# Kernel optimization log

Hardware: AMD Instinct MI355X
Metric: run time of the kernel (lower is better)

## Reference

```python
import jax, jax.numpy as jnp
import numpy as np
import math

NUM_HEADS = 16
HEAD_SIZE = 64
HIDDEN = NUM_HEADS * HEAD_SIZE
LN_EPS = 1e-12


def setup_inputs() -> dict:
    key = jax.random.key(0)
    ks = jax.random.split(key, 8)
    B, Lw, Le, H = 8, 512, 64, HIDDEN
    scale = 0.02
    return {
        "word_hidden_states": jax.random.normal(ks[0], (B, Lw, H), jnp.float32),
        "entity_hidden_states": jax.random.normal(ks[1], (B, Le, H), jnp.float32),
        "attention_mask": jnp.zeros((B, 1, 1, Lw + Le), jnp.float32),
        "Wq": jax.random.normal(ks[2], (H, H), jnp.float32) * scale,
        "bq": jnp.zeros((H,), jnp.float32),
        "Wk": jax.random.normal(ks[3], (H, H), jnp.float32) * scale,
        "bk": jnp.zeros((H,), jnp.float32),
        "Wv": jax.random.normal(ks[4], (H, H), jnp.float32) * scale,
        "bv": jnp.zeros((H,), jnp.float32),
        "Wo": jax.random.normal(ks[5], (H, H), jnp.float32) * scale,
        "bo": jnp.zeros((H,), jnp.float32),
        "ln_w": jnp.ones((H,), jnp.float32),
        "ln_b": jnp.zeros((H,), jnp.float32),
    }


def _layernorm(x, w, b):
    u = jnp.mean(x, axis=-1, keepdims=True)
    s = jnp.mean(jnp.square(x - u), axis=-1, keepdims=True)
    return w * ((x - u) / jnp.sqrt(s + LN_EPS)) + b


def reference(word_hidden_states, entity_hidden_states, attention_mask,
              Wq, bq, Wk, bk, Wv, bv, Wo, bo, ln_w, ln_b):
    B, Lw, H = word_hidden_states.shape
    x = jnp.concatenate([word_hidden_states, entity_hidden_states], axis=1)  # [B,S,H]
    S = x.shape[1]

    def heads(t):  # [B,S,H] -> [B,nh,S,hd]
        return t.reshape(B, S, NUM_HEADS, HEAD_SIZE).transpose(0, 2, 1, 3)

    q = heads(x @ Wq + bq)
    k = heads(x @ Wk + bk)
    v = heads(x @ Wv + bv)

    scores = jnp.einsum("bhqd,bhkd->bhqk", q, k) / math.sqrt(HEAD_SIZE)
    scores = scores + attention_mask  # additive mask, broadcast [B,1,1,S]
    probs = jax.nn.softmax(scores, axis=-1)
    ctx = jnp.einsum("bhqk,bhkd->bhqd", probs, v)
    ctx = ctx.transpose(0, 2, 1, 3).reshape(B, S, H)

    # SelfOutput (shared weights) applied per-stream; equivalent on concat since
    # residual is the concatenated input and LayerNorm is per-token.
    out = _layernorm(ctx @ Wo + bo + x, ln_w, ln_b)
    return out[:, :Lw, :], out[:, Lw:, :]
```

## Files before the change

### kernel.cpp

```cpp
#include <hip/hip_runtime.h>

#define NHEADS 16
#define HDIM   64
#define HID    1024
#define BATCH  8
#define LW     512
#define LE     64
#define SEQ    576
#define MTOT   (BATCH * SEQ)

typedef unsigned short u16;
typedef __bf16 bf16x8 __attribute__((ext_vector_type(8)));
typedef float  f32x4  __attribute__((ext_vector_type(4)));

__device__ __forceinline__ u16 f2bf(float f) {
  union { float f; unsigned int i; } x;
  x.f = f;
  unsigned int u = x.i;
  unsigned int r = (u + 0x7FFFu + ((u >> 16) & 1u)) >> 16;
  return (u16)r;
}
__device__ __forceinline__ unsigned int pk2(float a, float b) {
  return (unsigned int)f2bf(a) | ((unsigned int)f2bf(b) << 16);
}

__device__ __forceinline__ void gload16(const u16* g, u16* l) {
  __builtin_amdgcn_global_load_lds(
      (const __attribute__((address_space(1))) void*)g,
      (__attribute__((address_space(3))) void*)l, 16, 0, 0);
}

__global__ __launch_bounds__(256) void prep_k(
    const float* __restrict__ w0, const float* __restrict__ w1,
    const float* __restrict__ w2, const float* __restrict__ w3,
    u16* __restrict__ wt,
    const float* __restrict__ word, const float* __restrict__ ent,
    u16* __restrict__ xb)
{
  const int bid = blockIdx.x, tid = threadIdx.x;
  if (bid < 4096) {
    __shared__ u16 tile[32][33];
    const int z = bid >> 10, rem = bid & 1023;
    const int bx = rem & 31, by = rem >> 5;
    const float* src = (z == 0) ? w0 : (z == 1) ? w1 : (z == 2) ? w2 : w3;
    u16* dst = wt + (size_t)z * HID * HID;
    const int tx = tid & 31, ty = tid >> 5;
    const int nx = bx * 32, ky = by * 32;
#pragma unroll
    for (int j = 0; j < 4; ++j)
      tile[ty * 4 + j][tx] = f2bf(src[(size_t)(ky + ty * 4 + j) * HID + nx + tx]);
    __syncthreads();
#pragma unroll
    for (int j = 0; j < 4; ++j)
      dst[(size_t)(nx + ty * 4 + j) * HID + ky + tx] = tile[tx][ty * 4 + j];
  } else {
    const int row = bid - 4096;
    const int bb = row / SEQ, ss = row - bb * SEQ;
    const float* src = (ss < LW) ? word + (size_t)(bb * LW + ss) * HID
                                 : ent  + (size_t)(bb * LE + (ss - LW)) * HID;
    float4 v = *(const float4*)(src + tid * 4);
    ushort4 o;
    o.x = f2bf(v.x); o.y = f2bf(v.y); o.z = f2bf(v.z); o.w = f2bf(v.w);
    *(ushort4*)(xb + (size_t)row * HID + tid * 4) = o;
  }
}

__global__ __launch_bounds__(256) void qkv_gemm_k(
    const u16* __restrict__ xb, const u16* __restrict__ wt,
    const float* __restrict__ bq, const float* __restrict__ bk, const float* __restrict__ bv,
    u16* __restrict__ q_ws, u16* __restrict__ k_ws, u16* __restrict__ v_ws)
{
  __shared__ u16 sh[4 * 64 * 68];
  const int which = blockIdx.z;
  const u16* W = wt + (size_t)which * HID * HID;
  const float* bias = (which == 0) ? bq : (which == 1) ? bk : bv;
  const int m0 = blockIdx.x * 128, n0 = blockIdx.y * 128;
  const int tid = threadIdx.x, lane = tid & 63, wv = tid >> 6;
  const int lr = lane & 15, quad = lane >> 4;
  const int wm = (wv >> 1) * 64, wn = (wv & 1) * 64;

  const int subrow = lane >> 3;
  const int gsw = ((lane & 7) ^ subrow) * 8;
  const int fsw = lr & 7;

  u16* As = sh;
  u16* Bs = sh + 8192;

  const f32x4 fz = {0.f, 0.f, 0.f, 0.f};
  f32x4 acc[4][4];
#pragma unroll
  for (int a = 0; a < 4; ++a)
#pragma unroll
    for (int b = 0; b < 4; ++b) acc[a][b] = fz;

  for (int ki = 0; ki < 16; ++ki) {
    const int k0 = ki * 64;
#pragma unroll
    for (int j = 0; j < 4; ++j) {
      int row = (wv * 4 + j) * 8 + subrow;
      u16* ldst = sh + ((wv * 4 + j) * 64 + lane) * 8;
      gload16(xb + (size_t)(m0 + row) * HID + k0 + gsw, ldst);
      gload16(W  + (size_t)(n0 + row) * HID + k0 + gsw, ldst + 8192);
    }
    __syncthreads();
#pragma unroll
    for (int ks = 0; ks < 2; ++ks) {
      bf16x8 af[4], bfr[4];
#pragma unroll
      for (int i = 0; i < 4; ++i) {
        af[i]  = *(const bf16x8*)(&As[(wm + i * 16 + lr) * 64 + (((ks * 4 + quad) ^ fsw) * 8)]);
        bfr[i] = *(const bf16x8*)(&Bs[(wn + i * 16 + lr) * 64 + (((ks * 4 + quad) ^ fsw) * 8)]);
      }
      if (which < 2) {
#pragma unroll
        for (int a = 0; a < 4; ++a)
#pragma unroll
          for (int b = 0; b < 4; ++b)
            acc[a][b] = __builtin_amdgcn_mfma_f32_16x16x32_bf16(bfr[a], af[b], acc[a][b], 0, 0, 0);
      } else {
#pragma unroll
        for (int a = 0; a < 4; ++a)
#pragma unroll
          for (int b = 0; b < 4; ++b)
            acc[a][b] = __builtin_amdgcn_mfma_f32_16x16x32_bf16(af[a], bfr[b], acc[a][b], 0, 0, 0);
      }
    }
    __syncthreads();
  }

  u16* tb = sh + wv * (64 * 68);
  const int head = (n0 + wn) >> 6;
  const int mbase = m0 + wm;
  const int bb = mbase / SEQ;
  const int ssb = mbase - bb * SEQ;

  if (which < 2) {
    float4 bias4[4];
#pragma unroll
    for (int ni = 0; ni < 4; ++ni)
      bias4[ni] = *(const float4*)(bias + n0 + wn + ni * 16 + quad * 4);
#pragma unroll
    for (int mi = 0; mi < 4; ++mi)
#pragma unroll
      for (int ni = 0; ni < 4; ++ni) {
        uint2 w2v;
        w2v.x = pk2(acc[ni][mi][0] + bias4[ni].x, acc[ni][mi][1] + bias4[ni].y);
        w2v.y = pk2(acc[ni][mi][2] + bias4[ni].z, acc[ni][mi][3] + bias4[ni].w);
        *(uint2*)(&tb[(mi * 16 + lr) * 68 + ni * 16 + quad * 4]) = w2v;
      }
    u16* drow = (which == 0 ? q_ws : k_ws)
              + ((size_t)(bb * NHEADS + head) * SEQ + ssb) * HDIM;
#pragma unroll
    for (int i = 0; i < 8; ++i) {
      int rrow = i * 8 + (lane >> 3);
      int seg = lane & 7;
      bf16x8 v8 = *(const bf16x8*)(&tb[rrow * 68 + seg * 8]);
      *(bf16x8*)(drow + (size_t)rrow * HDIM + seg * 8) = v8;
    }
  } else {
    float bcol[4];
#pragma unroll
    for (int ni = 0; ni < 4; ++ni) bcol[ni] = bias[n0 + wn + ni * 16 + lr];
#pragma unroll
    for (int mi = 0; mi < 4; ++mi)
#pragma unroll
      for (int ni = 0; ni < 4; ++ni) {
        uint2 w2v;
        w2v.x = pk2(acc[mi][ni][0] + bcol[ni], acc[mi][ni][1] + bcol[ni]);
        w2v.y = pk2(acc[mi][ni][2] + bcol[ni], acc[mi][ni][3] + bcol[ni]);
        *(uint2*)(&tb[(ni * 16 + lr) * 68 + (mi >> 1) * 32 + quad * 8 + (mi & 1) * 4]) = w2v;
      }
    u16* dcol = v_ws + ((size_t)(bb * NHEADS + head) * HDIM) * SEQ + ssb;
#pragma unroll
    for (int i = 0; i < 8; ++i) {
      int d = i * 8 + (lane >> 3);
      int seg = lane & 7;
      bf16x8 v8 = *(const bf16x8*)(&tb[d * 68 + seg * 8]);
      *(bf16x8*)(dcol + (size_t)d * SEQ + seg * 8) = v8;
    }
  }
}

__global__ __launch_bounds__(256) void attn_k(
    const u16* __restrict__ q_ws, const u16* __restrict__ k_ws,
    const u16* __restrict__ v_ws, const float* __restrict__ mask,
    u16* __restrict__ ctxh)
{
  __shared__ u16 Ks[2][4096];
  __shared__ u16 Vs[2][4096];
  __shared__ float ms[576];
  const int bhx = blockIdx.x, qt = blockIdx.y;
  const int b = bhx >> 4, h = bhx & 15;
  const int tid = threadIdx.x, lane = tid & 63, wv = tid >> 6;
  const int lr = lane & 15, quad = lane >> 4;
  const int q0 = qt * 64 + wv * 16;
  const u16* kbh = k_ws + (size_t)bhx * SEQ * HDIM;
  const u16* vbh = v_ws + (size_t)bhx * HDIM * SEQ;
  const u16* qp  = q_ws + ((size_t)bhx * SEQ + q0) * HDIM;
  const float* mrow = mask + b * SEQ;

  if (tid < 144) *(float4*)(&ms[tid * 4]) = *(const float4*)(mrow + tid * 4);

  const int subrow = lane >> 3;
  const int gsw = (lane & 7) ^ subrow;

  bf16x8 qf[2];
  qf[0] = *(const bf16x8*)(qp + lr * HDIM + quad * 8);
  qf[1] = *(const bf16x8*)(qp + lr * HDIM + 32 + quad * 8);

  const f32x4 fz = {0.f, 0.f, 0.f, 0.f};
  f32x4 oa[4] = {fz, fz, fz, fz};
  f32x4 rsv = fz;
  const int fA = lr & 7;

#pragma unroll
  for (int j = 0; j < 2; ++j) {
    int row = (wv * 2 + j) * 8 + subrow;
    gload16(kbh + (size_t)row * HDIM + gsw * 8, &Ks[0][((wv * 2 + j) * 64 + lane) * 8]);
    gload16(vbh + (size_t)row * SEQ + gsw * 8,  &Vs[0][((wv * 2 + j) * 64 + lane) * 8]);
  }

  for (int ci = 0; ci < 9; ++ci) {
    const int cur = ci & 1;
    const int c = ci * 64;
    __syncthreads();
    if (ci + 1 < 9) {
      int cn = c + 64;
#pragma unroll
      for (int j = 0; j < 2; ++j) {
        int row = (wv * 2 + j) * 8 + subrow;
        gload16(kbh + ((size_t)(cn + row)) * HDIM + gsw * 8,
                &Ks[cur ^ 1][((wv * 2 + j) * 64 + lane) * 8]);
        gload16(vbh + (size_t)row * SEQ + cn + gsw * 8,
                &Vs[cur ^ 1][((wv * 2 + j) * 64 + lane) * 8]);
      }
    }
    f32x4 s[4] = {fz, fz, fz, fz};
#pragma unroll
    for (int ks = 0; ks < 2; ++ks)
#pragma unroll
      for (int t = 0; t < 4; ++t) {
        bf16x8 kf = *(const bf16x8*)(&Ks[cur][(t * 16 + lr) * 64 + (((ks * 4 + quad) ^ fA) * 8)]);
        s[t] = __builtin_amdgcn_mfma_f32_16x16x32_bf16(kf, qf[ks], s[t], 0, 0, 0);
      }
    unsigned int pk0[4], pk1[4];
#pragma unroll
    for (int t = 0; t < 4; ++t) {
      float4 mv = *(const float4*)(&ms[c + t * 16 + quad * 4]);
      s[t][0] = __expf(s[t][0] * 0.125f + mv.x);
      s[t][1] = __expf(s[t][1] * 0.125f + mv.y);
      s[t][2] = __expf(s[t][2] * 0.125f + mv.z);
      s[t][3] = __expf(s[t][3] * 0.125f + mv.w);
      rsv += s[t];
      pk0[t] = pk2(s[t][0], s[t][1]);
      pk1[t] = pk2(s[t][2], s[t][3]);
    }
#pragma unroll
    for (int ks = 0; ks < 2; ++ks) {
      union { unsigned int u[4]; bf16x8 v; } ap;
      ap.u[0] = pk0[ks * 2];     ap.u[1] = pk1[ks * 2];
      ap.u[2] = pk0[ks * 2 + 1]; ap.u[3] = pk1[ks * 2 + 1];
#pragma unroll
      for (int n = 0; n < 4; ++n) {
        bf16x8 vf = *(const bf16x8*)(&Vs[cur][(n * 16 + lr) * 64 + (((ks * 4 + quad) ^ fA) * 8)]);
        oa[n] = __builtin_amdgcn_mfma_f32_16x16x32_bf16(ap.v, vf, oa[n], 0, 0, 0);
      }
    }
  }

  float rl = rsv[0] + rsv[1] + rsv[2] + rsv[3];
  rl += __shfl_xor(rl, 16);
  rl += __shfl_xor(rl, 32);
  float inv = 1.0f / rl;
  float invr[4];
#pragma unroll
  for (int r = 0; r < 4; ++r) invr[r] = __shfl(inv, quad * 4 + r);

  u16* pw = (wv < 2) ? &Ks[1][wv * 2048] : &Vs[1][(wv - 2) * 2048];
#pragma unroll
  for (int n = 0; n < 4; ++n)
#pragma unroll
    for (int r = 0; r < 4; ++r)
      pw[(quad * 4 + r) * 68 + n * 16 + lr] = f2bf(oa[n][r] * invr[r]);
  const int token0 = b * SEQ + q0;
  u16* cb = ctxh + ((size_t)h * MTOT + token0) * HDIM;
#pragma unroll
  for (int i = 0; i < 2; ++i) {
    int row = lane & 15;
    int seg = (lane >> 4) + i * 4;
    bf16x8 v8 = *(const bf16x8*)(&pw[row * 68 + seg * 8]);
    *(bf16x8*)(cb + (size_t)row * HDIM + seg * 8) = v8;
  }
}

__global__ __launch_bounds__(256) void out_gemm_k(
    const u16* __restrict__ ctxh, const u16* __restrict__ wto,
    const float* __restrict__ bo,
    const float* __restrict__ word, const float* __restrict__ ent,
    float* __restrict__ y)
{
  __shared__ u16 sh[16384];
  const int m0 = blockIdx.x * 128, n0 = blockIdx.y * 128;
  const int tid = threadIdx.x, lane = tid & 63, wv = tid >> 6;
  const int lr = lane & 15, quad = lane >> 4;
  const int wm = (wv >> 1) * 64, wn = (wv & 1) * 64;
  const int subrow = lane >> 3;
  const int gsw = ((lane & 7) ^ subrow) * 8;
  const int fsw = lr & 7;
  u16* As = sh;
  u16* Bs = sh + 8192;

  const f32x4 fz = {0.f, 0.f, 0.f, 0.f};
  f32x4 acc[4][4];
#pragma unroll
  for (int mi = 0; mi < 4; ++mi)
#pragma unroll
    for (int ni = 0; ni < 4; ++ni) acc[mi][ni] = fz;

  for (int hb = 0; hb < 16; ++hb) {
#pragma unroll
    for (int j = 0; j < 4; ++j) {
      int row = (wv * 4 + j) * 8 + subrow;
      u16* ldst = sh + ((wv * 4 + j) * 64 + lane) * 8;
      gload16(ctxh + ((size_t)hb * MTOT + (m0 + row)) * HDIM + gsw, ldst);
      gload16(wto + (size_t)(n0 + row) * HID + hb * 64 + gsw, ldst + 8192);
    }
    __syncthreads();
#pragma unroll
    for (int ks = 0; ks < 2; ++ks) {
      bf16x8 af[4], bfr[4];
#pragma unroll
      for (int i = 0; i < 4; ++i) {
        af[i]  = *(const bf16x8*)(&As[(wm + i * 16 + lr) * 64 + (((ks * 4 + quad) ^ fsw) * 8)]);
        bfr[i] = *(const bf16x8*)(&Bs[(wn + i * 16 + lr) * 64 + (((ks * 4 + quad) ^ fsw) * 8)]);
      }
#pragma unroll
      for (int mi = 0; mi < 4; ++mi)
#pragma unroll
        for (int ni = 0; ni < 4; ++ni)
          acc[mi][ni] = __builtin_amdgcn_mfma_f32_16x16x32_bf16(af[mi], bfr[ni], acc[mi][ni], 0, 0, 0);
    }
    __syncthreads();
  }

#pragma unroll
  for (int mi = 0; mi < 4; ++mi) {
    int rowb = m0 + wm + mi * 16 + quad * 4;
#pragma unroll
    for (int r = 0; r < 4; ++r) {
      int row = rowb + r;
      int bb = row / SEQ, ss = row - bb * SEQ;
      const float* res = (ss < LW) ? (word + (size_t)(bb * LW + ss) * HID)
                                   : (ent  + (size_t)(bb * LE + (ss - LW)) * HID);
#pragma unroll
      for (int ni = 0; ni < 4; ++ni) {
        int col = n0 + wn + ni * 16 + lr;
        y[(size_t)row * HID + col] = acc[mi][ni][r] + bo[col] + res[col];
      }
    }
  }
}

__global__ __launch_bounds__(256) void ln_k(
    const float* __restrict__ y, const float* __restrict__ lnw,
    const float* __restrict__ lnb, float* __restrict__ out)
{
  const int row = blockIdx.x;
  const int tid = threadIdx.x;
  __shared__ float ssum[4], sqq[4];

  const float* yr = y + (size_t)row * HID;
  float4 v = *(const float4*)(yr + tid * 4);
  float s = v.x + v.y + v.z + v.w;
  float q = v.x * v.x + v.y * v.y + v.z * v.z + v.w * v.w;
#pragma unroll
  for (int o = 32; o > 0; o >>= 1) { s += __shfl_xor(s, o); q += __shfl_xor(q, o); }
  if ((tid & 63) == 0) { ssum[tid >> 6] = s; sqq[tid >> 6] = q; }
  __syncthreads();
  s = ssum[0] + ssum[1] + ssum[2] + ssum[3];
  q = sqq[0] + sqq[1] + sqq[2] + sqq[3];
  float mean = s * (1.0f / HID);
  float var  = q * (1.0f / HID) - mean * mean;
  float rstd = rsqrtf(var + 1e-12f);

  int bb = row / SEQ, ss2 = row - bb * SEQ;
  float* dst = (ss2 < LW)
             ? out + (size_t)(bb * LW + ss2) * HID
             : out + (size_t)BATCH * LW * HID + (size_t)(bb * LE + (ss2 - LW)) * HID;

  float4 w4 = *(const float4*)(lnw + tid * 4);
  float4 b4 = *(const float4*)(lnb + tid * 4);
  float4 o4;
  o4.x = w4.x * (v.x - mean) * rstd + b4.x;
  o4.y = w4.y * (v.y - mean) * rstd + b4.y;
  o4.z = w4.z * (v.z - mean) * rstd + b4.z;
  o4.w = w4.w * (v.w - mean) * rstd + b4.w;
  *(float4*)(dst + tid * 4) = o4;
}

extern "C" void kernel_launch(void* const* d_in, const int* in_sizes, int n_in,
                              void* d_out, int out_size, void* d_ws, size_t ws_size,
                              hipStream_t stream) {
  const float* word = (const float*)d_in[0];
  const float* ent  = (const float*)d_in[1];
  const float* mask = (const float*)d_in[2];
  const float* Wq   = (const float*)d_in[3];
  const float* bq   = (const float*)d_in[4];
  const float* Wk   = (const float*)d_in[5];
  const float* bk   = (const float*)d_in[6];
  const float* Wv   = (const float*)d_in[7];
  const float* bv   = (const float*)d_in[8];
  const float* Wo   = (const float*)d_in[9];
  const float* bo   = (const float*)d_in[10];
  const float* lnw  = (const float*)d_in[11];
  const float* lnb  = (const float*)d_in[12];

  char* base = (char*)d_ws;
  u16*   wt   = (u16*)base;
  u16*   q_ws = (u16*)(base + (size_t)8 * 1024 * 1024);
  u16*   k_ws = q_ws + (size_t)MTOT * HID;
  u16*   v_ws = k_ws + (size_t)MTOT * HID;
  u16*   ctxh = v_ws + (size_t)MTOT * HID;
  char*  xy   = (char*)(ctxh + (size_t)MTOT * HID);
  u16*   xb   = (u16*)xy;
  float* y    = (float*)xy;

  hipLaunchKernelGGL(prep_k, dim3(4096 + MTOT), dim3(256), 0, stream,
                     Wq, Wk, Wv, Wo, wt, word, ent, xb);
  hipLaunchKernelGGL(qkv_gemm_k, dim3(MTOT / 128, HID / 128, 3), dim3(256), 0, stream,
                     xb, wt, bq, bk, bv, q_ws, k_ws, v_ws);
  hipLaunchKernelGGL(attn_k, dim3(BATCH * NHEADS, SEQ / 64), dim3(256), 0, stream,
                     q_ws, k_ws, v_ws, mask, ctxh);
  hipLaunchKernelGGL(out_gemm_k, dim3(MTOT / 128, HID / 128), dim3(256), 0, stream,
                     ctxh, wt + (size_t)3 * HID * HID, bo, word, ent, y);
  hipLaunchKernelGGL(ln_k, dim3(MTOT), dim3(256), 0, stream,
                     y, lnw, lnb, (float*)d_out);
}
```

Before: 202.4 us.

## Shrink GEMM tiles for more blocks and drop attention double buffering

Result: slower. 211.3 us (+4.4%).

```diff
diff --git a/kernel.cpp b/kernel.cpp
--- a/kernel.cpp
+++ b/kernel.cpp
@@ -70,112 +70,119 @@
     const float* __restrict__ bq, const float* __restrict__ bk, const float* __restrict__ bv,
     u16* __restrict__ q_ws, u16* __restrict__ k_ws, u16* __restrict__ v_ws)
 {
-  __shared__ u16 sh[4 * 64 * 68];
+  __shared__ u16 sh[12288];
+  u16* As = sh;
+  u16* Bs = sh + 4096;
   const int which = blockIdx.z;
   const u16* W = wt + (size_t)which * HID * HID;
   const float* bias = (which == 0) ? bq : (which == 1) ? bk : bv;
-  const int m0 = blockIdx.x * 128, n0 = blockIdx.y * 128;
+  const int m0 = blockIdx.x * 64, n0 = blockIdx.y * 128;
   const int tid = threadIdx.x, lane = tid & 63, wv = tid >> 6;
   const int lr = lane & 15, quad = lane >> 4;
-  const int wm = (wv >> 1) * 64, wn = (wv & 1) * 64;
+  const int wn = wv * 32;
 
   const int subrow = lane >> 3;
   const int gsw = ((lane & 7) ^ subrow) * 8;
   const int fsw = lr & 7;
 
-  u16* As = sh;
-  u16* Bs = sh + 8192;
-
   const f32x4 fz = {0.f, 0.f, 0.f, 0.f};
-  f32x4 acc[4][4];
-#pragma unroll
-  for (int a = 0; a < 4; ++a)
-#pragma unroll
-    for (int b = 0; b < 4; ++b) acc[a][b] = fz;
+  f32x4 acc[8];
+#pragma unroll
+  for (int i = 0; i < 8; ++i) acc[i] = fz;
 
   for (int ki = 0; ki < 16; ++ki) {
     const int k0 = ki * 64;
 #pragma unroll
+    for (int j = 0; j < 2; ++j) {
+      int row = (wv * 2 + j) * 8 + subrow;
+      gload16(xb + (size_t)(m0 + row) * HID + k0 + gsw,
+              As + ((wv * 2 + j) * 64 + lane) * 8);
+    }
+#pragma unroll
     for (int j = 0; j < 4; ++j) {
       int row = (wv * 4 + j) * 8 + subrow;
-      u16* ldst = sh + ((wv * 4 + j) * 64 + lane) * 8;
-      gload16(xb + (size_t)(m0 + row) * HID + k0 + gsw, ldst);
-      gload16(W  + (size_t)(n0 + row) * HID + k0 + gsw, ldst + 8192);
+      gload16(W + (size_t)(n0 + row) * HID + k0 + gsw,
+              Bs + ((wv * 4 + j) * 64 + lane) * 8);
     }
     __syncthreads();
 #pragma unroll
     for (int ks = 0; ks < 2; ++ks) {
-      bf16x8 af[4], bfr[4];
-#pragma unroll
-      for (int i = 0; i < 4; ++i) {
-        af[i]  = *(const bf16x8*)(&As[(wm + i * 16 + lr) * 64 + (((ks * 4 + quad) ^ fsw) * 8)]);
-        bfr[i] = *(const bf16x8*)(&Bs[(wn + i * 16 + lr) * 64 + (((ks * 4 + quad) ^ fsw) * 8)]);
-      }
+      const int kc = (((ks * 4 + quad) ^ fsw) * 8);
+      bf16x8 af[4], bfr[2];
+#pragma unroll
+      for (int i = 0; i < 4; ++i)
+        af[i] = *(const bf16x8*)(&As[(i * 16 + lr) * 64 + kc]);
+#pragma unroll
+      for (int i = 0; i < 2; ++i)
+        bfr[i] = *(const bf16x8*)(&Bs[(wn + i * 16 + lr) * 64 + kc]);
       if (which < 2) {
 #pragma unroll
-        for (int a = 0; a < 4; ++a)
+        for (int a = 0; a < 2; ++a)
 #pragma unroll
           for (int b = 0; b < 4; ++b)
-            acc[a][b] = __builtin_amdgcn_mfma_f32_16x16x32_bf16(bfr[a], af[b], acc[a][b], 0, 0, 0);
+            acc[a * 4 + b] = __builtin_amdgcn_mfma_f32_16x16x32_bf16(bfr[a], af[b], acc[a * 4 + b], 0, 0, 0);
       } else {
 #pragma unroll
-        for (int a = 0; a < 4; ++a)
-#pragma unroll
-          for (int b = 0; b < 4; ++b)
-            acc[a][b] = __builtin_amdgcn_mfma_f32_16x16x32_bf16(af[a], bfr[b], acc[a][b], 0, 0, 0);
-      }
-    }
-    __syncthreads();
-  }
-
-  u16* tb = sh + wv * (64 * 68);
-  const int head = (n0 + wn) >> 6;
-  const int mbase = m0 + wm;
-  const int bb = mbase / SEQ;
-  const int ssb = mbase - bb * SEQ;
+        for (int mi = 0; mi < 4; ++mi)
+#pragma unroll
+          for (int ni = 0; ni < 2; ++ni)
+            acc[mi * 2 + ni] = __builtin_amdgcn_mfma_f32_16x16x32_bf16(af[mi], bfr[ni], acc[mi * 2 + ni], 0, 0, 0);
+      }
+    }
+    __syncthreads();
+  }
+
+  const int hl = wn >> 6;
+  const int wnh = wn & 63;
+  u16* tg = sh + hl * (64 * 68);
+  const int bb = m0 / SEQ, ssb = m0 - bb * SEQ;
+  const int headg = (n0 >> 6) + hl;
+  const int sub = wv & 1;
 
   if (which < 2) {
-    float4 bias4[4];
-#pragma unroll
-    for (int ni = 0; ni < 4; ++ni)
-      bias4[ni] = *(const float4*)(bias + n0 + wn + ni * 16 + quad * 4);
+    float4 bias4[2];
+#pragma unroll
+    for (int a = 0; a < 2; ++a)
+      bias4[a] = *(const float4*)(bias + n0 + wn + a * 16 + quad * 4);
+#pragma unroll
+    for (int b = 0; b < 4; ++b)
+#pragma unroll
+      for (int a = 0; a < 2; ++a) {
+        uint2 w2v;
+        w2v.x = pk2(acc[a * 4 + b][0] + bias4[a].x, acc[a * 4 + b][1] + bias4[a].y);
+        w2v.y = pk2(acc[a * 4 + b][2] + bias4[a].z, acc[a * 4 + b][3] + bias4[a].w);
+        *(uint2*)(&tg[(b * 16 + lr) * 68 + wnh + a * 16 + quad * 4]) = w2v;
+      }
+    __syncthreads();
+    u16* drow = (which == 0 ? q_ws : k_ws)
+              + ((size_t)(bb * NHEADS + headg) * SEQ + ssb) * HDIM;
+#pragma unroll
+    for (int i = 0; i < 4; ++i) {
+      int rrow = sub * 32 + i * 8 + (lane >> 3);
+      int seg = lane & 7;
+      bf16x8 v8 = *(const bf16x8*)(&tg[rrow * 68 + seg * 8]);
+      *(bf16x8*)(drow + (size_t)rrow * HDIM + seg * 8) = v8;
+    }
+  } else {
+    float bcol[2];
+#pragma unroll
+    for (int ni = 0; ni < 2; ++ni) bcol[ni] = bias[n0 + wn + ni * 16 + lr];
 #pragma unroll
     for (int mi = 0; mi < 4; ++mi)
 #pragma unroll
-      for (int ni = 0; ni < 4; ++ni) {
+      for (int ni = 0; ni < 2; ++ni) {
         uint2 w2v;
-        w2v.x = pk2(acc[ni][mi][0] + bias4[ni].x, acc[ni][mi][1] + bias4[ni].y);
-        w2v.y = pk2(acc[ni][mi][2] + bias4[ni].z, acc[ni][mi][3] + bias4[ni].w);
-        *(uint2*)(&tb[(mi * 16 + lr) * 68 + ni * 16 + quad * 4]) = w2v;
-      }
-    u16* drow = (which == 0 ? q_ws : k_ws)
-              + ((size_t)(bb * NHEADS + head) * SEQ + ssb) * HDIM;
-#pragma unroll
-    for (int i = 0; i < 8; ++i) {
-      int rrow = i * 8 + (lane >> 3);
+        w2v.x = pk2(acc[mi * 2 + ni][0] + bcol[ni], acc[mi * 2 + ni][1] + bcol[ni]);
+        w2v.y = pk2(acc[mi * 2 + ni][2] + bcol[ni], acc[mi * 2 + ni][3] + bcol[ni]);
+        *(uint2*)(&tg[(wnh + ni * 16 + lr) * 68 + (mi >> 1) * 32 + quad * 8 + (mi & 1) * 4]) = w2v;
+      }
+    __syncthreads();
+    u16* dcol = v_ws + ((size_t)(bb * NHEADS + headg) * HDIM) * SEQ + ssb;
+#pragma unroll
+    for (int i = 0; i < 4; ++i) {
+      int d = sub * 32 + i * 8 + (lane >> 3);
       int seg = lane & 7;
-      bf16x8 v8 = *(const bf16x8*)(&tb[rrow * 68 + seg * 8]);
-      *(bf16x8*)(drow + (size_t)rrow * HDIM + seg * 8) = v8;
-    }
-  } else {
-    float bcol[4];
-#pragma unroll
-    for (int ni = 0; ni < 4; ++ni) bcol[ni] = bias[n0 + wn + ni * 16 + lr];
-#pragma unroll
-    for (int mi = 0; mi < 4; ++mi)
-#pragma unroll
-      for (int ni = 0; ni < 4; ++ni) {
-        uint2 w2v;
-        w2v.x = pk2(acc[mi][ni][0] + bcol[ni], acc[mi][ni][1] + bcol[ni]);
-        w2v.y = pk2(acc[mi][ni][2] + bcol[ni], acc[mi][ni][3] + bcol[ni]);
-        *(uint2*)(&tb[(ni * 16 + lr) * 68 + (mi >> 1) * 32 + quad * 8 + (mi & 1) * 4]) = w2v;
-      }
-    u16* dcol = v_ws + ((size_t)(bb * NHEADS + head) * HDIM) * SEQ + ssb;
-#pragma unroll
-    for (int i = 0; i < 8; ++i) {
-      int d = i * 8 + (lane >> 3);
-      int seg = lane & 7;
-      bf16x8 v8 = *(const bf16x8*)(&tb[d * 68 + seg * 8]);
+      bf16x8 v8 = *(const bf16x8*)(&tg[d * 68 + seg * 8]);
       *(bf16x8*)(dcol + (size_t)d * SEQ + seg * 8) = v8;
     }
   }
@@ -186,8 +193,8 @@
     const u16* __restrict__ v_ws, const float* __restrict__ mask,
     u16* __restrict__ ctxh)
 {
-  __shared__ u16 Ks[2][4096];
-  __shared__ u16 Vs[2][4096];
+  __shared__ u16 Ks[4096];
+  __shared__ u16 Vs[4096];
   __shared__ float ms[576];
   const int bhx = blockIdx.x, qt = blockIdx.y;
   const int b = bhx >> 4, h = bhx & 15;
@@ -213,34 +220,23 @@
   f32x4 rsv = fz;
   const int fA = lr & 7;
 
-#pragma unroll
-  for (int j = 0; j < 2; ++j) {
-    int row = (wv * 2 + j) * 8 + subrow;
-    gload16(kbh + (size_t)row * HDIM + gsw * 8, &Ks[0][((wv * 2 + j) * 64 + lane) * 8]);
-    gload16(vbh + (size_t)row * SEQ + gsw * 8,  &Vs[0][((wv * 2 + j) * 64 + lane) * 8]);
-  }
-
   for (int ci = 0; ci < 9; ++ci) {
-    const int cur = ci & 1;
     const int c = ci * 64;
-    __syncthreads();
-    if (ci + 1 < 9) {
-      int cn = c + 64;
-#pragma unroll
-      for (int j = 0; j < 2; ++j) {
-        int row = (wv * 2 + j) * 8 + subrow;
-        gload16(kbh + ((size_t)(cn + row)) * HDIM + gsw * 8,
-                &Ks[cur ^ 1][((wv * 2 + j) * 64 + lane) * 8]);
-        gload16(vbh + (size_t)row * SEQ + cn + gsw * 8,
-                &Vs[cur ^ 1][((wv * 2 + j) * 64 + lane) * 8]);
-      }
-    }
+#pragma unroll
+    for (int j = 0; j < 2; ++j) {
+      int row = (wv * 2 + j) * 8 + subrow;
+      gload16(kbh + ((size_t)(c + row)) * HDIM + gsw * 8,
+              &Ks[((wv * 2 + j) * 64 + lane) * 8]);
+      gload16(vbh + (size_t)row * SEQ + c + gsw * 8,
+              &Vs[((wv * 2 + j) * 64 + lane) * 8]);
+    }
+    __syncthreads();
     f32x4 s[4] = {fz, fz, fz, fz};
 #pragma unroll
     for (int ks = 0; ks < 2; ++ks)
 #pragma unroll
       for (int t = 0; t < 4; ++t) {
-        bf16x8 kf = *(const bf16x8*)(&Ks[cur][(t * 16 + lr) * 64 + (((ks * 4 + quad) ^ fA) * 8)]);
+        bf16x8 kf = *(const bf16x8*)(&Ks[(t * 16 + lr) * 64 + (((ks * 4 + quad) ^ fA) * 8)]);
         s[t] = __builtin_amdgcn_mfma_f32_16x16x32_bf16(kf, qf[ks], s[t], 0, 0, 0);
       }
     unsigned int pk0[4], pk1[4];
@@ -262,10 +258,11 @@
       ap.u[2] = pk0[ks * 2 + 1]; ap.u[3] = pk1[ks * 2 + 1];
 #pragma unroll
       for (int n = 0; n < 4; ++n) {
-        bf16x8 vf = *(const bf16x8*)(&Vs[cur][(n * 16 + lr) * 64 + (((ks * 4 + quad) ^ fA) * 8)]);
+        bf16x8 vf = *(const bf16x8*)(&Vs[(n * 16 + lr) * 64 + (((ks * 4 + quad) ^ fA) * 8)]);
         oa[n] = __builtin_amdgcn_mfma_f32_16x16x32_bf16(ap.v, vf, oa[n], 0, 0, 0);
       }
     }
+    __syncthreads();
   }
 
   float rl = rsv[0] + rsv[1] + rsv[2] + rsv[3];
@@ -276,7 +273,7 @@
 #pragma unroll
   for (int r = 0; r < 4; ++r) invr[r] = __shfl(inv, quad * 4 + r);
 
-  u16* pw = (wv < 2) ? &Ks[1][wv * 2048] : &Vs[1][(wv - 2) * 2048];
+  u16* pw = (wv < 2) ? &Ks[wv * 2048] : &Vs[(wv - 2) * 2048];
 #pragma unroll
   for (int n = 0; n < 4; ++n)
 #pragma unroll
@@ -299,53 +296,58 @@
     const float* __restrict__ word, const float* __restrict__ ent,
     float* __restrict__ y)
 {
-  __shared__ u16 sh[16384];
-  const int m0 = blockIdx.x * 128, n0 = blockIdx.y * 128;
+  __shared__ u16 sh[10240];
+  u16* As = sh;
+  u16* Bs = sh + 2048;
+  const int m0 = blockIdx.x * 32, n0 = blockIdx.y * 128;
   const int tid = threadIdx.x, lane = tid & 63, wv = tid >> 6;
   const int lr = lane & 15, quad = lane >> 4;
-  const int wm = (wv >> 1) * 64, wn = (wv & 1) * 64;
+  const int wn = wv * 32;
   const int subrow = lane >> 3;
   const int gsw = ((lane & 7) ^ subrow) * 8;
   const int fsw = lr & 7;
-  u16* As = sh;
-  u16* Bs = sh + 8192;
 
   const f32x4 fz = {0.f, 0.f, 0.f, 0.f};
-  f32x4 acc[4][4];
-#pragma unroll
-  for (int mi = 0; mi < 4; ++mi)
-#pragma unroll
-    for (int ni = 0; ni < 4; ++ni) acc[mi][ni] = fz;
+  f32x4 acc[2][2];
+#pragma unroll
+  for (int mi = 0; mi < 2; ++mi)
+#pragma unroll
+    for (int ni = 0; ni < 2; ++ni) acc[mi][ni] = fz;
 
   for (int hb = 0; hb < 16; ++hb) {
+    {
+      int row = wv * 8 + subrow;
+      gload16(ctxh + ((size_t)hb * MTOT + (m0 + row)) * HDIM + gsw,
+              As + (wv * 64 + lane) * 8);
+    }
 #pragma unroll
     for (int j = 0; j < 4; ++j) {
       int row = (wv * 4 + j) * 8 + subrow;
-      u16* ldst = sh + ((wv * 4 + j) * 64 + lane) * 8;
-      gload16(ctxh + ((size_t)hb * MTOT + (m0 + row)) * HDIM + gsw, ldst);
-      gload16(wto + (size_t)(n0 + row) * HID + hb * 64 + gsw, ldst + 8192);
+      gload16(wto + (size_t)(n0 + row) * HID + hb * 64 + gsw,
+              Bs + ((wv * 4 + j) * 64 + lane) * 8);
     }
     __syncthreads();
 #pragma unroll
     for (int ks = 0; ks < 2; ++ks) {
-      bf16x8 af[4], bfr[4];
-#pragma unroll
-      for (int i = 0; i < 4; ++i) {
-        af[i]  = *(const bf16x8*)(&As[(wm + i * 16 + lr) * 64 + (((ks * 4 + quad) ^ fsw) * 8)]);
-        bfr[i] = *(const bf16x8*)(&Bs[(wn + i * 16 + lr) * 64 + (((ks * 4 + quad) ^ fsw) * 8)]);
-      }
-#pragma unroll
-      for (int mi = 0; mi < 4; ++mi)
-#pragma unroll
-        for (int ni = 0; ni < 4; ++ni)
+      const int kc = (((ks * 4 + quad) ^ fsw) * 8);
+      bf16x8 af[2], bfr[2];
+#pragma unroll
+      for (int i = 0; i < 2; ++i) {
+        af[i]  = *(const bf16x8*)(&As[(i * 16 + lr) * 64 + kc]);
+        bfr[i] = *(const bf16x8*)(&Bs[(wn + i * 16 + lr) * 64 + kc]);
+      }
+#pragma unroll
+      for (int mi = 0; mi < 2; ++mi)
+#pragma unroll
+        for (int ni = 0; ni < 2; ++ni)
           acc[mi][ni] = __builtin_amdgcn_mfma_f32_16x16x32_bf16(af[mi], bfr[ni], acc[mi][ni], 0, 0, 0);
     }
     __syncthreads();
   }
 
 #pragma unroll
-  for (int mi = 0; mi < 4; ++mi) {
-    int rowb = m0 + wm + mi * 16 + quad * 4;
+  for (int mi = 0; mi < 2; ++mi) {
+    int rowb = m0 + mi * 16 + quad * 4;
 #pragma unroll
     for (int r = 0; r < 4; ++r) {
       int row = rowb + r;
@@ -353,7 +355,7 @@
       const float* res = (ss < LW) ? (word + (size_t)(bb * LW + ss) * HID)
                                    : (ent  + (size_t)(bb * LE + (ss - LW)) * HID);
 #pragma unroll
-      for (int ni = 0; ni < 4; ++ni) {
+      for (int ni = 0; ni < 2; ++ni) {
         int col = n0 + wn + ni * 16 + lr;
         y[(size_t)row * HID + col] = acc[mi][ni][r] + bo[col] + res[col];
       }
@@ -427,11 +429,11 @@
 
   hipLaunchKernelGGL(prep_k, dim3(4096 + MTOT), dim3(256), 0, stream,
                      Wq, Wk, Wv, Wo, wt, word, ent, xb);
-  hipLaunchKernelGGL(qkv_gemm_k, dim3(MTOT / 128, HID / 128, 3), dim3(256), 0, stream,
+  hipLaunchKernelGGL(qkv_gemm_k, dim3(MTOT / 64, HID / 128, 3), dim3(256), 0, stream,
                      xb, wt, bq, bk, bv, q_ws, k_ws, v_ws);
   hipLaunchKernelGGL(attn_k, dim3(BATCH * NHEADS, SEQ / 64), dim3(256), 0, stream,
                      q_ws, k_ws, v_ws, mask, ctxh);
-  hipLaunchKernelGGL(out_gemm_k, dim3(MTOT / 128, HID / 128), dim3(256), 0, stream,
+  hipLaunchKernelGGL(out_gemm_k, dim3(MTOT / 32, HID / 128), dim3(256), 0, stream,
                      ctxh, wt + (size_t)3 * HID * HID, bo, word, ent, y);
   hipLaunchKernelGGL(ln_k, dim3(MTOT), dim3(256), 0, stream,
                      y, lnw, lnb, (float*)d_out);
```

## Single-buffer attention K/V tiles and shrink output GEMM M-tile to 32

Applied to the files above, without the earlier changes.

Measured after the change: 195.7 us. 1.03x faster.

```diff
diff --git a/kernel.cpp b/kernel.cpp
--- a/kernel.cpp
+++ b/kernel.cpp
@@ -186,8 +186,8 @@
     const u16* __restrict__ v_ws, const float* __restrict__ mask,
     u16* __restrict__ ctxh)
 {
-  __shared__ u16 Ks[2][4096];
-  __shared__ u16 Vs[2][4096];
+  __shared__ u16 Ks[4096];
+  __shared__ u16 Vs[4096];
   __shared__ float ms[576];
   const int bhx = blockIdx.x, qt = blockIdx.y;
   const int b = bhx >> 4, h = bhx & 15;
@@ -213,34 +213,23 @@
   f32x4 rsv = fz;
   const int fA = lr & 7;
 
-#pragma unroll
-  for (int j = 0; j < 2; ++j) {
-    int row = (wv * 2 + j) * 8 + subrow;
-    gload16(kbh + (size_t)row * HDIM + gsw * 8, &Ks[0][((wv * 2 + j) * 64 + lane) * 8]);
-    gload16(vbh + (size_t)row * SEQ + gsw * 8,  &Vs[0][((wv * 2 + j) * 64 + lane) * 8]);
-  }
-
   for (int ci = 0; ci < 9; ++ci) {
-    const int cur = ci & 1;
     const int c = ci * 64;
-    __syncthreads();
-    if (ci + 1 < 9) {
-      int cn = c + 64;
-#pragma unroll
-      for (int j = 0; j < 2; ++j) {
-        int row = (wv * 2 + j) * 8 + subrow;
-        gload16(kbh + ((size_t)(cn + row)) * HDIM + gsw * 8,
-                &Ks[cur ^ 1][((wv * 2 + j) * 64 + lane) * 8]);
-        gload16(vbh + (size_t)row * SEQ + cn + gsw * 8,
-                &Vs[cur ^ 1][((wv * 2 + j) * 64 + lane) * 8]);
-      }
-    }
+#pragma unroll
+    for (int j = 0; j < 2; ++j) {
+      int row = (wv * 2 + j) * 8 + subrow;
+      gload16(kbh + ((size_t)(c + row)) * HDIM + gsw * 8,
+              &Ks[((wv * 2 + j) * 64 + lane) * 8]);
+      gload16(vbh + (size_t)row * SEQ + c + gsw * 8,
+              &Vs[((wv * 2 + j) * 64 + lane) * 8]);
+    }
+    __syncthreads();
     f32x4 s[4] = {fz, fz, fz, fz};
 #pragma unroll
     for (int ks = 0; ks < 2; ++ks)
 #pragma unroll
       for (int t = 0; t < 4; ++t) {
-        bf16x8 kf = *(const bf16x8*)(&Ks[cur][(t * 16 + lr) * 64 + (((ks * 4 + quad) ^ fA) * 8)]);
+        bf16x8 kf = *(const bf16x8*)(&Ks[(t * 16 + lr) * 64 + (((ks * 4 + quad) ^ fA) * 8)]);
         s[t] = __builtin_amdgcn_mfma_f32_16x16x32_bf16(kf, qf[ks], s[t], 0, 0, 0);
       }
     unsigned int pk0[4], pk1[4];
@@ -262,10 +251,11 @@
       ap.u[2] = pk0[ks * 2 + 1]; ap.u[3] = pk1[ks * 2 + 1];
 #pragma unroll
       for (int n = 0; n < 4; ++n) {
-        bf16x8 vf = *(const bf16x8*)(&Vs[cur][(n * 16 + lr) * 64 + (((ks * 4 + quad) ^ fA) * 8)]);
+        bf16x8 vf = *(const bf16x8*)(&Vs[(n * 16 + lr) * 64 + (((ks * 4 + quad) ^ fA) * 8)]);
         oa[n] = __builtin_amdgcn_mfma_f32_16x16x32_bf16(ap.v, vf, oa[n], 0, 0, 0);
       }
     }
+    __syncthreads();
   }
 
   float rl = rsv[0] + rsv[1] + rsv[2] + rsv[3];
@@ -276,7 +266,7 @@
 #pragma unroll
   for (int r = 0; r < 4; ++r) invr[r] = __shfl(inv, quad * 4 + r);
 
-  u16* pw = (wv < 2) ? &Ks[1][wv * 2048] : &Vs[1][(wv - 2) * 2048];
+  u16* pw = (wv < 2) ? &Ks[wv * 2048] : &Vs[(wv - 2) * 2048];
 #pragma unroll
   for (int n = 0; n < 4; ++n)
 #pragma unroll
@@ -299,53 +289,58 @@
     const float* __restrict__ word, const float* __restrict__ ent,
     float* __restrict__ y)
 {
-  __shared__ u16 sh[16384];
-  const int m0 = blockIdx.x * 128, n0 = blockIdx.y * 128;
+  __shared__ u16 sh[10240];
+  u16* As = sh;
+  u16* Bs = sh + 2048;
+  const int m0 = blockIdx.x * 32, n0 = blockIdx.y * 128;
   const int tid = threadIdx.x, lane = tid & 63, wv = tid >> 6;
   const int lr = lane & 15, quad = lane >> 4;
-  const int wm = (wv >> 1) * 64, wn = (wv & 1) * 64;
+  const int wn = wv * 32;
   const int subrow = lane >> 3;
   const int gsw = ((lane & 7) ^ subrow) * 8;
   const int fsw = lr & 7;
-  u16* As = sh;
-  u16* Bs = sh + 8192;
 
   const f32x4 fz = {0.f, 0.f, 0.f, 0.f};
-  f32x4 acc[4][4];
-#pragma unroll
-  for (int mi = 0; mi < 4; ++mi)
-#pragma unroll
-    for (int ni = 0; ni < 4; ++ni) acc[mi][ni] = fz;
+  f32x4 acc[2][2];
+#pragma unroll
+  for (int mi = 0; mi < 2; ++mi)
+#pragma unroll
+    for (int ni = 0; ni < 2; ++ni) acc[mi][ni] = fz;
 
   for (int hb = 0; hb < 16; ++hb) {
+    {
+      int row = wv * 8 + subrow;
+      gload16(ctxh + ((size_t)hb * MTOT + (m0 + row)) * HDIM + gsw,
+              As + (wv * 64 + lane) * 8);
+    }
 #pragma unroll
     for (int j = 0; j < 4; ++j) {
       int row = (wv * 4 + j) * 8 + subrow;
-      u16* ldst = sh + ((wv * 4 + j) * 64 + lane) * 8;
-      gload16(ctxh + ((size_t)hb * MTOT + (m0 + row)) * HDIM + gsw, ldst);
-      gload16(wto + (size_t)(n0 + row) * HID + hb * 64 + gsw, ldst + 8192);
+      gload16(wto + (size_t)(n0 + row) * HID + hb * 64 + gsw,
+              Bs + ((wv * 4 + j) * 64 + lane) * 8);
     }
     __syncthreads();
 #pragma unroll
     for (int ks = 0; ks < 2; ++ks) {
-      bf16x8 af[4], bfr[4];
-#pragma unroll
-      for (int i = 0; i < 4; ++i) {
-        af[i]  = *(const bf16x8*)(&As[(wm + i * 16 + lr) * 64 + (((ks * 4 + quad) ^ fsw) * 8)]);
-        bfr[i] = *(const bf16x8*)(&Bs[(wn + i * 16 + lr) * 64 + (((ks * 4 + quad) ^ fsw) * 8)]);
-      }
-#pragma unroll
-      for (int mi = 0; mi < 4; ++mi)
-#pragma unroll
-        for (int ni = 0; ni < 4; ++ni)
+      const int kc = (((ks * 4 + quad) ^ fsw) * 8);
+      bf16x8 af[2], bfr[2];
+#pragma unroll
+      for (int i = 0; i < 2; ++i) {
+        af[i]  = *(const bf16x8*)(&As[(i * 16 + lr) * 64 + kc]);
+        bfr[i] = *(const bf16x8*)(&Bs[(wn + i * 16 + lr) * 64 + kc]);
+      }
+#pragma unroll
+      for (int mi = 0; mi < 2; ++mi)
+#pragma unroll
+        for (int ni = 0; ni < 2; ++ni)
           acc[mi][ni] = __builtin_amdgcn_mfma_f32_16x16x32_bf16(af[mi], bfr[ni], acc[mi][ni], 0, 0, 0);
     }
     __syncthreads();
   }
 
 #pragma unroll
-  for (int mi = 0; mi < 4; ++mi) {
-    int rowb = m0 + wm + mi * 16 + quad * 4;
+  for (int mi = 0; mi < 2; ++mi) {
+    int rowb = m0 + mi * 16 + quad * 4;
 #pragma unroll
     for (int r = 0; r < 4; ++r) {
       int row = rowb + r;
@@ -353,7 +348,7 @@
       const float* res = (ss < LW) ? (word + (size_t)(bb * LW + ss) * HID)
                                    : (ent  + (size_t)(bb * LE + (ss - LW)) * HID);
 #pragma unroll
-      for (int ni = 0; ni < 4; ++ni) {
+      for (int ni = 0; ni < 2; ++ni) {
         int col = n0 + wn + ni * 16 + lr;
         y[(size_t)row * HID + col] = acc[mi][ni][r] + bo[col] + res[col];
       }
@@ -431,7 +426,7 @@
                      xb, wt, bq, bk, bv, q_ws, k_ws, v_ws);
   hipLaunchKernelGGL(attn_k, dim3(BATCH * NHEADS, SEQ / 64), dim3(256), 0, stream,
                      q_ws, k_ws, v_ws, mask, ctxh);
-  hipLaunchKernelGGL(out_gemm_k, dim3(MTOT / 128, HID / 128), dim3(256), 0, stream,
+  hipLaunchKernelGGL(out_gemm_k, dim3(MTOT / 32, HID / 128), dim3(256), 0, stream,
                      ctxh, wt + (size_t)3 * HID * HID, bo, word, ent, y);
   hipLaunchKernelGGL(ln_k, dim3(MTOT), dim3(256), 0, stream,
                      y, lnw, lnb, (float*)d_out);
```
